# Kernel optimization log

Hardware: AMD Instinct MI355X
Metric: run time of the kernel (lower is better)

Reference implementation:

```python
import jax, jax.numpy as jnp
import numpy as np

B, C, H, W = 16, 64, 64, 64
N_CODES = 4096


def setup_inputs() -> dict:
    key = jax.random.key(0)
    k1, k2 = jax.random.split(key)
    z = jax.random.normal(k1, (B, C, H, W), dtype=jnp.float32)
    emb = jax.random.normal(k2, (N_CODES, C), dtype=jnp.float32)
    return {"z": z, "emb": emb}


def reference(z, emb):
    b, c, h, w = z.shape
    embf = emb.astype(jnp.float32)
    # (b, c, h, w) -> (N, c) flattened tokens
    zf = jnp.transpose(z, (0, 2, 3, 1)).reshape(-1, c).astype(jnp.float32)
    # squared L2 distances: ||z||^2 - 2 z.e + ||e||^2, shape (N, n_codes)
    d = (
        jnp.sum(zf * zf, axis=1, keepdims=True)
        - 2.0 * (zf @ embf.T)
        + jnp.sum(embf * embf, axis=1)
    )
    idx = jnp.argmin(d, axis=1)  # (N,)
    zq = embf[idx].reshape(b, h, w, c)
    zq = jnp.transpose(zq, (0, 3, 1, 2))
    return zq.astype(z.dtype)
```

## Files before the change

kernel.cpp:

```cpp
#include <hip/hip_runtime.h>


typedef __attribute__((ext_vector_type(8))) short short8;
typedef __attribute__((ext_vector_type(4))) float f32x4;
typedef unsigned int u32;
typedef __attribute__((address_space(3))) u32 lds_u32;
typedef const __attribute__((address_space(1))) u32 glb_u32;

#define NCHUNK 256
#define GROUP 4
#define NGROUP 64
#define FRAGS 6
#define CHUNK_BYTES (FRAGS * 64 * 16)
#define GROUP_BYTES (GROUP * CHUNK_BYTES)
#define WSB_BYTES (NCHUNK * CHUNK_BYTES)
#define WS_NEEDED ((size_t)WSB_BYTES + 16384u)

static __device__ __forceinline__ unsigned short f2bf(float f) {
    u32 u = __builtin_bit_cast(u32, f);
    u += 0x7fffu + ((u >> 16) & 1u);
    return (unsigned short)(u >> 16);
}
static __device__ __forceinline__ float bf2f(unsigned short h) {
    u32 u = ((u32)h) << 16;
    return __builtin_bit_cast(float, u);
}

__global__ void vq_norm_kernel(const float* __restrict__ emb, float* __restrict__ nrm) {
    int c = blockIdx.x * 256 + threadIdx.x;
    const float* e = emb + c * 64;
    float s = 0.f;
#pragma unroll
    for (int k = 0; k < 64; ++k) { float v = e[k]; s = fmaf(v, v, s); }
    nrm[c] = 0.5f * s;
}

__global__ void vq_pack_kernel(const float* __restrict__ emb, unsigned short* __restrict__ wsB) {
    int ck    = blockIdx.x;
    int f     = threadIdx.x >> 6;
    int lane  = threadIdx.x & 63;
    int level = f >> 1, s = f & 1;
    int code  = ck * 16 + (lane & 15);
    int kb    = s * 32 + (lane >> 4) * 8;
    const float* src = emb + code * 64 + kb;
    short8 o;
#pragma unroll
    for (int j = 0; j < 8; ++j) {
        float x = src[j];
        unsigned short h1 = f2bf(x);
        float r1 = x - bf2f(h1);
        unsigned short h2 = f2bf(r1);
        float r2 = r1 - bf2f(h2);
        unsigned short h3 = f2bf(r2);
        o[j] = (short)(level == 0 ? h1 : (level == 1 ? h2 : h3));
    }
    ((short8*)wsB)[(ck * FRAGS + f) * 64 + lane] = o;
}

__global__ __launch_bounds__(256, 2) void vq_main_kernel(
    const float* __restrict__ z, const float* __restrict__ emb,
    const unsigned short* __restrict__ wsB, const float* __restrict__ wsN,
    float* __restrict__ out)
{
    __shared__ char  sB[2][GROUP_BYTES];
    __shared__ float sN[2][64];
    __shared__ int   sBest[128];

    const int wave = threadIdx.x >> 6;
    const int lane = threadIdx.x & 63;
    const int quad = lane >> 4;
    const int col  = lane & 15;

    const int t0 = blockIdx.x * 128 + wave * 32;

    short8 a[2][3][2];
#pragma unroll
    for (int t = 0; t < 2; ++t) {
        const int tok = t0 + t * 16 + col;
        const int b   = tok >> 12;
        const int hw  = tok & 4095;
        const float* zp = z + b * 262144 + hw;
#pragma unroll
        for (int s = 0; s < 2; ++s)
#pragma unroll
            for (int j = 0; j < 8; ++j) {
                int k = s * 32 + quad * 8 + j;
                float x = zp[k * 4096];
                unsigned short h1 = f2bf(x);
                float r1 = x - bf2f(h1);
                unsigned short h2 = f2bf(r1);
                float r2 = r1 - bf2f(h2);
                a[t][0][s][j] = (short)h1;
                a[t][1][s][j] = (short)h2;
                a[t][2][s][j] = (short)f2bf(r2);
            }
    }

    float best[2][4];
    int   bidx[2][4];
#pragma unroll
    for (int t = 0; t < 2; ++t)
#pragma unroll
        for (int r = 0; r < 4; ++r) { best[t][r] = -3.4e38f; bidx[t][r] = 0; }

    auto stage = [&](int buf, int g) {
        const char* gbase = ((const char*)wsB) + g * GROUP_BYTES + wave * CHUNK_BYTES;
        char*       lbase = sB[buf] + wave * CHUNK_BYTES;
#pragma unroll
        for (int i = 0; i < 6; ++i)
            __builtin_amdgcn_global_load_lds(
                (glb_u32*)(gbase + i * 1024 + lane * 16),
                (lds_u32*)(lbase + i * 1024), 16, 0, 0);
        if (wave == 0)
            __builtin_amdgcn_global_load_lds(
                (glb_u32*)(wsN + g * 64 + lane),
                (lds_u32*)&sN[buf][0], 4, 0, 0);
    };

    stage(0, 0);

    for (int g = 0; g < NGROUP; ++g) {
        const int cur = g & 1;
        __syncthreads();
        if (g + 1 < NGROUP) stage(cur ^ 1, g + 1);

#pragma unroll
        for (int cl = 0; cl < GROUP; ++cl) {
            const int ck = g * GROUP + cl;
            const char* base = sB[cur] + cl * CHUNK_BYTES;
            short8 b10 = ((const short8*)(base + 0 * 1024))[lane];
            short8 b11 = ((const short8*)(base + 1 * 1024))[lane];
            short8 b20 = ((const short8*)(base + 2 * 1024))[lane];
            short8 b21 = ((const short8*)(base + 3 * 1024))[lane];
            short8 b30 = ((const short8*)(base + 4 * 1024))[lane];
            short8 b31 = ((const short8*)(base + 5 * 1024))[lane];
            const float nrm  = sN[cur][cl * 16 + col];
            const int   code = ck * 16 + col;

#pragma unroll
            for (int t = 0; t < 2; ++t) {
                f32x4 acc = {0.f, 0.f, 0.f, 0.f};
                acc = __builtin_amdgcn_mfma_f32_16x16x32_bf16(a[t][1][0], b20, acc, 0, 0, 0);
                acc = __builtin_amdgcn_mfma_f32_16x16x32_bf16(a[t][1][1], b21, acc, 0, 0, 0);
                acc = __builtin_amdgcn_mfma_f32_16x16x32_bf16(a[t][0][0], b30, acc, 0, 0, 0);
                acc = __builtin_amdgcn_mfma_f32_16x16x32_bf16(a[t][0][1], b31, acc, 0, 0, 0);
                acc = __builtin_amdgcn_mfma_f32_16x16x32_bf16(a[t][2][0], b10, acc, 0, 0, 0);
                acc = __builtin_amdgcn_mfma_f32_16x16x32_bf16(a[t][2][1], b11, acc, 0, 0, 0);
                acc = __builtin_amdgcn_mfma_f32_16x16x32_bf16(a[t][0][0], b20, acc, 0, 0, 0);
                acc = __builtin_amdgcn_mfma_f32_16x16x32_bf16(a[t][0][1], b21, acc, 0, 0, 0);
                acc = __builtin_amdgcn_mfma_f32_16x16x32_bf16(a[t][1][0], b10, acc, 0, 0, 0);
                acc = __builtin_amdgcn_mfma_f32_16x16x32_bf16(a[t][1][1], b11, acc, 0, 0, 0);
                acc = __builtin_amdgcn_mfma_f32_16x16x32_bf16(a[t][0][0], b10, acc, 0, 0, 0);
                acc = __builtin_amdgcn_mfma_f32_16x16x32_bf16(a[t][0][1], b11, acc, 0, 0, 0);

#pragma unroll
                for (int r = 0; r < 4; ++r) {
                    float score = acc[r] - nrm;
                    if (score > best[t][r]) { best[t][r] = score; bidx[t][r] = code; }
                }
            }
        }
    }

#pragma unroll
    for (int off = 1; off < 16; off <<= 1)
#pragma unroll
        for (int t = 0; t < 2; ++t)
#pragma unroll
            for (int r = 0; r < 4; ++r) {
                float os = __shfl_xor(best[t][r], off, 64);
                int   oi = __shfl_xor(bidx[t][r], off, 64);
                if (os > best[t][r] || (os == best[t][r] && oi < bidx[t][r])) {
                    best[t][r] = os; bidx[t][r] = oi;
                }
            }
    if (col == 0)
#pragma unroll
        for (int t = 0; t < 2; ++t)
#pragma unroll
            for (int r = 0; r < 4; ++r)
                sBest[wave * 32 + t * 16 + quad * 4 + r] = bidx[t][r];
    __syncthreads();

    const int tk   = threadIdx.x & 127;
    const int coff = (threadIdx.x >> 7) * 32;
    const int gt   = blockIdx.x * 128 + tk;
    const int ob   = gt >> 12, ohw = gt & 4095;
    float* op = out + ob * 262144 + ohw;
    const float4* ep = (const float4*)(emb + sBest[tk] * 64 + coff);
#pragma unroll
    for (int i = 0; i < 8; ++i) {
        float4 v = ep[i];
        op[(coff + 4 * i + 0) * 4096] = v.x;
        op[(coff + 4 * i + 1) * 4096] = v.y;
        op[(coff + 4 * i + 2) * 4096] = v.z;
        op[(coff + 4 * i + 3) * 4096] = v.w;
    }
}

__global__ __launch_bounds__(256) void vq_fp32_kernel(
    const float* __restrict__ z, const float* __restrict__ emb,
    float* __restrict__ out)
{
    __shared__ float se[64 * 64];
    __shared__ float snorm[64];

    const int t  = blockIdx.x * 256 + threadIdx.x;
    const int b  = t >> 12;
    const int hw = t & 4095;
    const float* zt = z + (size_t)b * 262144 + hw;
    float zf[64];
#pragma unroll
    for (int c = 0; c < 64; ++c) zf[c] = zt[(size_t)c * 4096];

    float best = -3.4e38f;
    int   bestIdx = 0;
    for (int k0 = 0; k0 < 4096; k0 += 64) {
        __syncthreads();
        const float4* src = (const float4*)(emb + (size_t)k0 * 64);
        float4*       dst = (float4*)se;
#pragma unroll
        for (int i = 0; i < 4; ++i)
            dst[i * 256 + threadIdx.x] = src[i * 256 + threadIdx.x];
        __syncthreads();
        if (threadIdx.x < 64) {
            float s = 0.f;
#pragma unroll
            for (int c = 0; c < 64; ++c) {
                float v = se[threadIdx.x * 64 + c];
                s = fmaf(v, v, s);
            }
            snorm[threadIdx.x] = 0.5f * s;
        }
        __syncthreads();
#pragma unroll 4
        for (int kk = 0; kk < 64; ++kk) {
            float dot = 0.f;
#pragma unroll
            for (int c = 0; c < 64; ++c)
                dot = fmaf(zf[c], se[kk * 64 + c], dot);
            float score = dot - snorm[kk];
            if (score > best) { best = score; bestIdx = k0 + kk; }
        }
    }
    const float* e  = emb + (size_t)bestIdx * 64;
    float*       ot = out + (size_t)b * 262144 + hw;
#pragma unroll
    for (int c = 0; c < 64; ++c) ot[(size_t)c * 4096] = e[c];
}

extern "C" void kernel_launch(void* const* d_in, const int* in_sizes, int n_in,
                              void* d_out, int out_size, void* d_ws, size_t ws_size,
                              hipStream_t stream) {
    const float* z   = (const float*)d_in[0];
    const float* emb = (const float*)d_in[1];
    float*       out = (float*)d_out;

    if (ws_size < WS_NEEDED) {
        vq_fp32_kernel<<<256, 256, 0, stream>>>(z, emb, out);
        return;
    }

    unsigned short* wsB = (unsigned short*)d_ws;
    float*          wsN = (float*)((char*)d_ws + WSB_BYTES);

    vq_norm_kernel<<<16, 256, 0, stream>>>(emb, wsN);
    vq_pack_kernel<<<256, 384, 0, stream>>>(emb, wsB);
    vq_main_kernel<<<512, 256, 0, stream>>>(z, emb, wsB, wsN, out);
}
```

Before: 220.4 us.

## Use two-term fp16 split with near-tie fp32 rescoring pass

Replaces the three-term bf16 split (6 MFMA products per chunk) with a two-term fp16 split using 3 products, which halves the MFMA work and cuts the staged B bytes. Each token also tracks its second-best score; tokens whose top-two margin is under a fixed delta go into a global list via atomics. A new fix kernel recomputes those tokens exactly in fp32 and rewrites their output. The norm kernel is folded into the pack kernel. This adds a third launch and an atomic counter, and correctness depends on the fixed delta covering the fp16 error.

```diff
diff --git a/kernel.cpp b/kernel.cpp
--- a/kernel.cpp
+++ b/kernel.cpp
@@ -1,8 +1,9 @@
 #include <hip/hip_runtime.h>
 
 
-typedef __attribute__((ext_vector_type(8))) short short8;
-typedef __attribute__((ext_vector_type(4))) float f32x4;
+typedef __attribute__((ext_vector_type(8))) short    short8;
+typedef __attribute__((ext_vector_type(8))) _Float16 half8;
+typedef __attribute__((ext_vector_type(4))) float    f32x4;
 typedef unsigned int u32;
 typedef __attribute__((address_space(3))) u32 lds_u32;
 typedef const __attribute__((address_space(1))) u32 glb_u32;
@@ -10,32 +11,20 @@
 #define NCHUNK 256
 #define GROUP 4
 #define NGROUP 64
-#define FRAGS 6
+#define FRAGS 4
 #define CHUNK_BYTES (FRAGS * 64 * 16)
 #define GROUP_BYTES (GROUP * CHUNK_BYTES)
 #define WSB_BYTES (NCHUNK * CHUNK_BYTES)
-#define WS_NEEDED ((size_t)WSB_BYTES + 16384u)
-
-static __device__ __forceinline__ unsigned short f2bf(float f) {
-    u32 u = __builtin_bit_cast(u32, f);
-    u += 0x7fffu + ((u >> 16) & 1u);
-    return (unsigned short)(u >> 16);
-}
-static __device__ __forceinline__ float bf2f(unsigned short h) {
-    u32 u = ((u32)h) << 16;
-    return __builtin_bit_cast(float, u);
-}
-
-__global__ void vq_norm_kernel(const float* __restrict__ emb, float* __restrict__ nrm) {
-    int c = blockIdx.x * 256 + threadIdx.x;
-    const float* e = emb + c * 64;
-    float s = 0.f;
-#pragma unroll
-    for (int k = 0; k < 64; ++k) { float v = e[k]; s = fmaf(v, v, s); }
-    nrm[c] = 0.5f * s;
-}
-
-__global__ void vq_pack_kernel(const float* __restrict__ emb, unsigned short* __restrict__ wsB) {
+#define OFF_N    WSB_BYTES
+#define OFF_CNT  (OFF_N + 16384)
+#define OFF_LIST (OFF_CNT + 64)
+#define WS_NEEDED ((size_t)OFF_LIST + 65536u * 4u)
+#define DELTA 0.005f
+
+__global__ void vq_pack_kernel(const float* __restrict__ emb,
+                               unsigned short* __restrict__ wsB,
+                               float* __restrict__ wsN,
+                               u32* __restrict__ wsCnt) {
     int ck    = blockIdx.x;
     int f     = threadIdx.x >> 6;
     int lane  = threadIdx.x & 63;
@@ -47,19 +36,27 @@
 #pragma unroll
     for (int j = 0; j < 8; ++j) {
         float x = src[j];
-        unsigned short h1 = f2bf(x);
-        float r1 = x - bf2f(h1);
-        unsigned short h2 = f2bf(r1);
-        float r2 = r1 - bf2f(h2);
-        unsigned short h3 = f2bf(r2);
-        o[j] = (short)(level == 0 ? h1 : (level == 1 ? h2 : h3));
+        _Float16 h1 = (_Float16)x;
+        _Float16 h2 = (_Float16)(x - (float)h1);
+        o[j] = __builtin_bit_cast(short, level == 0 ? h1 : h2);
     }
     ((short8*)wsB)[(ck * FRAGS + f) * 64 + lane] = o;
+
+    if (threadIdx.x < 16) {
+        int c = ck * 16 + threadIdx.x;
+        const float* e = emb + c * 64;
+        float ssum = 0.f;
+#pragma unroll
+        for (int k = 0; k < 64; ++k) { float v = e[k]; ssum = fmaf(v, v, ssum); }
+        wsN[c] = 0.5f * ssum;
+    }
+    if (ck == 0 && threadIdx.x == 0) *wsCnt = 0u;
 }
 
 __global__ __launch_bounds__(256, 2) void vq_main_kernel(
     const float* __restrict__ z, const float* __restrict__ emb,
     const unsigned short* __restrict__ wsB, const float* __restrict__ wsN,
+    u32* __restrict__ wsCnt, u32* __restrict__ wsList,
     float* __restrict__ out)
 {
     __shared__ char  sB[2][GROUP_BYTES];
@@ -73,7 +70,7 @@
 
     const int t0 = blockIdx.x * 128 + wave * 32;
 
-    short8 a[2][3][2];
+    half8 a[2][2][2];
 #pragma unroll
     for (int t = 0; t < 2; ++t) {
         const int tok = t0 + t * 16 + col;
@@ -86,28 +83,26 @@
             for (int j = 0; j < 8; ++j) {
                 int k = s * 32 + quad * 8 + j;
                 float x = zp[k * 4096];
-                unsigned short h1 = f2bf(x);
-                float r1 = x - bf2f(h1);
-                unsigned short h2 = f2bf(r1);
-                float r2 = r1 - bf2f(h2);
-                a[t][0][s][j] = (short)h1;
-                a[t][1][s][j] = (short)h2;
-                a[t][2][s][j] = (short)f2bf(r2);
-            }
-    }
-
-    float best[2][4];
+                _Float16 h1 = (_Float16)x;
+                a[t][0][s][j] = h1;
+                a[t][1][s][j] = (_Float16)(x - (float)h1);
+            }
+    }
+
+    float best[2][4], best2[2][4];
     int   bidx[2][4];
 #pragma unroll
     for (int t = 0; t < 2; ++t)
 #pragma unroll
-        for (int r = 0; r < 4; ++r) { best[t][r] = -3.4e38f; bidx[t][r] = 0; }
+        for (int r = 0; r < 4; ++r) {
+            best[t][r] = -3.4e38f; best2[t][r] = -3.4e38f; bidx[t][r] = 0;
+        }
 
     auto stage = [&](int buf, int g) {
         const char* gbase = ((const char*)wsB) + g * GROUP_BYTES + wave * CHUNK_BYTES;
         char*       lbase = sB[buf] + wave * CHUNK_BYTES;
 #pragma unroll
-        for (int i = 0; i < 6; ++i)
+        for (int i = 0; i < 4; ++i)
             __builtin_amdgcn_global_load_lds(
                 (glb_u32*)(gbase + i * 1024 + lane * 16),
                 (lds_u32*)(lbase + i * 1024), 16, 0, 0);
@@ -128,35 +123,29 @@
         for (int cl = 0; cl < GROUP; ++cl) {
             const int ck = g * GROUP + cl;
             const char* base = sB[cur] + cl * CHUNK_BYTES;
-            short8 b10 = ((const short8*)(base + 0 * 1024))[lane];
-            short8 b11 = ((const short8*)(base + 1 * 1024))[lane];
-            short8 b20 = ((const short8*)(base + 2 * 1024))[lane];
-            short8 b21 = ((const short8*)(base + 3 * 1024))[lane];
-            short8 b30 = ((const short8*)(base + 4 * 1024))[lane];
-            short8 b31 = ((const short8*)(base + 5 * 1024))[lane];
+            half8 b10 = __builtin_bit_cast(half8, ((const short8*)(base + 0 * 1024))[lane]);
+            half8 b11 = __builtin_bit_cast(half8, ((const short8*)(base + 1 * 1024))[lane]);
+            half8 b20 = __builtin_bit_cast(half8, ((const short8*)(base + 2 * 1024))[lane]);
+            half8 b21 = __builtin_bit_cast(half8, ((const short8*)(base + 3 * 1024))[lane]);
             const float nrm  = sN[cur][cl * 16 + col];
             const int   code = ck * 16 + col;
 
 #pragma unroll
             for (int t = 0; t < 2; ++t) {
                 f32x4 acc = {0.f, 0.f, 0.f, 0.f};
-                acc = __builtin_amdgcn_mfma_f32_16x16x32_bf16(a[t][1][0], b20, acc, 0, 0, 0);
-                acc = __builtin_amdgcn_mfma_f32_16x16x32_bf16(a[t][1][1], b21, acc, 0, 0, 0);
-                acc = __builtin_amdgcn_mfma_f32_16x16x32_bf16(a[t][0][0], b30, acc, 0, 0, 0);
-                acc = __builtin_amdgcn_mfma_f32_16x16x32_bf16(a[t][0][1], b31, acc, 0, 0, 0);
-                acc = __builtin_amdgcn_mfma_f32_16x16x32_bf16(a[t][2][0], b10, acc, 0, 0, 0);
-                acc = __builtin_amdgcn_mfma_f32_16x16x32_bf16(a[t][2][1], b11, acc, 0, 0, 0);
-                acc = __builtin_amdgcn_mfma_f32_16x16x32_bf16(a[t][0][0], b20, acc, 0, 0, 0);
-                acc = __builtin_amdgcn_mfma_f32_16x16x32_bf16(a[t][0][1], b21, acc, 0, 0, 0);
-                acc = __builtin_amdgcn_mfma_f32_16x16x32_bf16(a[t][1][0], b10, acc, 0, 0, 0);
-                acc = __builtin_amdgcn_mfma_f32_16x16x32_bf16(a[t][1][1], b11, acc, 0, 0, 0);
-                acc = __builtin_amdgcn_mfma_f32_16x16x32_bf16(a[t][0][0], b10, acc, 0, 0, 0);
-                acc = __builtin_amdgcn_mfma_f32_16x16x32_bf16(a[t][0][1], b11, acc, 0, 0, 0);
+                acc = __builtin_amdgcn_mfma_f32_16x16x32_f16(a[t][1][0], b10, acc, 0, 0, 0);
+                acc = __builtin_amdgcn_mfma_f32_16x16x32_f16(a[t][1][1], b11, acc, 0, 0, 0);
+                acc = __builtin_amdgcn_mfma_f32_16x16x32_f16(a[t][0][0], b20, acc, 0, 0, 0);
+                acc = __builtin_amdgcn_mfma_f32_16x16x32_f16(a[t][0][1], b21, acc, 0, 0, 0);
+                acc = __builtin_amdgcn_mfma_f32_16x16x32_f16(a[t][0][0], b10, acc, 0, 0, 0);
+                acc = __builtin_amdgcn_mfma_f32_16x16x32_f16(a[t][0][1], b11, acc, 0, 0, 0);
 
 #pragma unroll
                 for (int r = 0; r < 4; ++r) {
-                    float score = acc[r] - nrm;
-                    if (score > best[t][r]) { best[t][r] = score; bidx[t][r] = code; }
+                    float sc  = acc[r] - nrm;
+                    bool  gt1 = sc > best[t][r];
+                    best2[t][r] = gt1 ? best[t][r] : fmaxf(sc, best2[t][r]);
+                    if (gt1) { best[t][r] = sc; bidx[t][r] = code; }
                 }
             }
         }
@@ -168,18 +157,28 @@
         for (int t = 0; t < 2; ++t)
 #pragma unroll
             for (int r = 0; r < 4; ++r) {
-                float os = __shfl_xor(best[t][r], off, 64);
-                int   oi = __shfl_xor(bidx[t][r], off, 64);
-                if (os > best[t][r] || (os == best[t][r] && oi < bidx[t][r])) {
-                    best[t][r] = os; bidx[t][r] = oi;
+                float os1 = __shfl_xor(best[t][r],  off, 64);
+                int   oi1 = __shfl_xor(bidx[t][r],  off, 64);
+                float os2 = __shfl_xor(best2[t][r], off, 64);
+                bool take = (os1 > best[t][r]) ||
+                            (os1 == best[t][r] && oi1 < bidx[t][r]);
+                float ns2 = take ? fmaxf(best[t][r], os2)
+                                 : fmaxf(best2[t][r], os1);
+                if (take) { best[t][r] = os1; bidx[t][r] = oi1; }
+                best2[t][r] = ns2;
+            }
+    if (col == 0)
+#pragma unroll
+        for (int t = 0; t < 2; ++t)
+#pragma unroll
+            for (int r = 0; r < 4; ++r) {
+                int tokb = wave * 32 + t * 16 + quad * 4 + r;
+                sBest[tokb] = bidx[t][r];
+                if (best[t][r] - best2[t][r] < DELTA) {
+                    u32 slot = atomicAdd(wsCnt, 1u);
+                    wsList[slot] = (u32)(blockIdx.x * 128 + tokb);
                 }
             }
-    if (col == 0)
-#pragma unroll
-        for (int t = 0; t < 2; ++t)
-#pragma unroll
-            for (int r = 0; r < 4; ++r)
-                sBest[wave * 32 + t * 16 + quad * 4 + r] = bidx[t][r];
     __syncthreads();
 
     const int tk   = threadIdx.x & 127;
@@ -198,6 +197,43 @@
     }
 }
 
+__global__ __launch_bounds__(256) void vq_fix_kernel(
+    const float* __restrict__ z, const float* __restrict__ emb,
+    const float* __restrict__ wsN, const u32* __restrict__ wsCnt,
+    const u32* __restrict__ wsList, float* __restrict__ out)
+{
+    const int nw   = gridDim.x * 4;
+    const int wid  = blockIdx.x * 4 + (threadIdx.x >> 6);
+    const int lane = threadIdx.x & 63;
+    const u32 count = *wsCnt;
+
+    for (u32 u = wid; u < count; u += nw) {
+        const int t  = (int)wsList[u];
+        const int b  = t >> 12, hw = t & 4095;
+        const float* zp = z + b * 262144 + hw;
+        float zf[64];
+#pragma unroll
+        for (int c = 0; c < 64; ++c) zf[c] = zp[c * 4096];
+
+        float best = -3.4e38f; int bi = 0;
+        for (int k = lane; k < 4096; k += 64) {
+            const float* e = emb + k * 64;
+            float dot = 0.f;
+#pragma unroll
+            for (int c = 0; c < 64; ++c) dot = fmaf(zf[c], e[c], dot);
+            float score = dot - wsN[k];
+            if (score > best) { best = score; bi = k; }
+        }
+#pragma unroll
+        for (int off = 1; off < 64; off <<= 1) {
+            float os = __shfl_xor(best, off, 64);
+            int   oi = __shfl_xor(bi,   off, 64);
+            if (os > best || (os == best && oi < bi)) { best = os; bi = oi; }
+        }
+        out[b * 262144 + lane * 4096 + hw] = emb[bi * 64 + lane];
+    }
+}
+
 __global__ __launch_bounds__(256) void vq_fp32_kernel(
     const float* __restrict__ z, const float* __restrict__ emb,
     float* __restrict__ out)
@@ -261,10 +297,12 @@
         return;
     }
 
-    unsigned short* wsB = (unsigned short*)d_ws;
-    float*          wsN = (float*)((char*)d_ws + WSB_BYTES);
-
-    vq_norm_kernel<<<16, 256, 0, stream>>>(emb, wsN);
-    vq_pack_kernel<<<256, 384, 0, stream>>>(emb, wsB);
-    vq_main_kernel<<<512, 256, 0, stream>>>(z, emb, wsB, wsN, out);
-}
+    unsigned short* wsB   = (unsigned short*)d_ws;
+    float*          wsN   = (float*)((char*)d_ws + OFF_N);
+    u32*            wsCnt = (u32*)((char*)d_ws + OFF_CNT);
+    u32*            wsList= (u32*)((char*)d_ws + OFF_LIST);
+
+    vq_pack_kernel<<<256, 256, 0, stream>>>(emb, wsB, wsN, wsCnt);
+    vq_main_kernel<<<512, 256, 0, stream>>>(z, emb, wsB, wsN, wsCnt, wsList, out);
+    vq_fix_kernel<<<256, 256, 0, stream>>>(z, emb, wsN, wsCnt, wsList, out);
+}
```

After: 314.0 us. 1.42x slower.
